# Optimization experiments

Hardware: AMD Instinct MI355X
Metric: run time of the kernel (lower is better)

## Reference

```python
import jax, jax.numpy as jnp
import numpy as np

B, L, D = 8, 2048, 512


def setup_inputs() -> dict:
    key = jax.random.key(0)
    ks = jax.random.split(key, 6)
    s = 0.02
    return {
        "q": jax.random.normal(ks[0], (B, L, D), jnp.float32),
        "k": jax.random.normal(ks[1], (B, L, D), jnp.float32),
        "v": jax.random.normal(ks[2], (B, L, D), jnp.float32),
        "Wq": jax.random.normal(ks[3], (D, D), jnp.float32) * s,
        "bq": jnp.zeros((D,), jnp.float32),
        "Wk": jax.random.normal(ks[4], (D, D), jnp.float32) * s,
        "bk": jnp.zeros((D,), jnp.float32),
        "Wv": jax.random.normal(ks[5], (D, D), jnp.float32) * s,
        "bv": jnp.zeros((D,), jnp.float32),
    }


def reference(q, k, v, Wq, bq, Wk, bk, Wv, bv):
    # Linear projections (torch Linear: x @ W.T + b)
    qp = jnp.einsum("bld,ed->ble", q, Wq) + bq
    kp = jnp.einsum("bld,ed->ble", k, Wk) + bk
    vp = jnp.einsum("bld,ed->ble", v, Wv) + bv
    # attn[b, i, j] = qp[b, i] . kp[b, j]   (no 1/sqrt(d) scaling in source)
    attn = jnp.einsum("bqd,bkd->bqk", qp, kp)
    # Faithful to torch.nn.Softmax(dim=1): normalize over the QUERY axis.
    attn = jax.nn.softmax(attn, axis=1)
    out = jnp.einsum("bqk,bkd->bqd", attn, vp)
    return out
```

## Files before the change

kernel.cpp:

```cpp
#include <hip/hip_runtime.h>
#include <math.h>


#define TKK 32

typedef __attribute__((ext_vector_type(8))) short bf16x8;
typedef __attribute__((ext_vector_type(4))) float floatx4;

typedef __attribute__((address_space(3))) short lds_short;
typedef const __attribute__((address_space(1))) short glob_short;

__device__ __forceinline__ short f2bf(float x) {
    unsigned u = __float_as_uint(x);
    u += 0x7fff + ((u >> 16) & 1);
    return (short)(u >> 16);
}
__device__ __forceinline__ float bf2f(short s) {
    return __uint_as_float(((unsigned)(unsigned short)s) << 16);
}
__device__ __forceinline__ float exp2_fast(float x) {
    float r;
    asm("v_exp_f32 %0, %1" : "=v"(r) : "v"(x));
    return r;
}

#define STAGE_SC(lane) ((((lane) & 3) ^ (((lane) >> 3) & 3)) * 8)
#define FRAG_FC(lane) (((((lane) >> 4) ^ (((lane) >> 1) & 3))) * 8)

__global__ __launch_bounds__(256) void prep(
    const float* __restrict__ q, const float* __restrict__ k,
    const float* __restrict__ v,
    const float* __restrict__ Wq, const float* __restrict__ Wk,
    const float* __restrict__ Wv,
    short* __restrict__ q_bf, short* __restrict__ k_bf, short* __restrict__ v_bf,
    short* __restrict__ Wq_bf, short* __restrict__ Wk_bf, short* __restrict__ Wv_bf,
    float* __restrict__ colsum)
{
    const int b = blockIdx.x;
    const float* in = nullptr;
    short* out = nullptr;
    long long i;
    if (b < 12288) {
        const int z = b >> 12;
        in  = (z == 0) ? q    : (z == 1) ? k    : v;
        out = (z == 0) ? q_bf : (z == 1) ? k_bf : v_bf;
        i = ((long long)(b & 4095) * 256 + threadIdx.x) * 8;
    } else if (b < 12672) {
        const int z = (b - 12288) >> 7;
        in  = (z == 0) ? Wq    : (z == 1) ? Wk    : Wv;
        out = (z == 0) ? Wq_bf : (z == 1) ? Wk_bf : Wv_bf;
        i = ((long long)((b - 12288) & 127) * 256 + threadIdx.x) * 8;
    } else {
        colsum[(b - 12672) * 256 + threadIdx.x] = 0.f;
        return;
    }
    float4 x = *(const float4*)(in + i);
    float4 y = *(const float4*)(in + i + 4);
    bf16x8 r;
    r[0] = f2bf(x.x); r[1] = f2bf(x.y); r[2] = f2bf(x.z); r[3] = f2bf(x.w);
    r[4] = f2bf(y.x); r[5] = f2bf(y.y); r[6] = f2bf(y.z); r[7] = f2bf(y.w);
    *(bf16x8*)(out + i) = r;
}

template<int TMp, int TNp, int WM, int WN, int HAS_BIAS, int OUT_BF16>
__device__ __forceinline__ void gemm_body(
    const short* __restrict__ A, const short* __restrict__ B,
    const float* __restrict__ bias, void* __restrict__ C,
    int N, int K, int m0, int n0, float escale)
{
    __shared__ short As[TMp * TKK];
    __shared__ short Bs[TNp * TKK];
    constexpr int MI = TMp / (16 * WM);
    constexpr int NJ = TNp / (16 * WN);
    const int t    = threadIdx.x;
    const int wave = t >> 6;
    const int lane = t & 63;
    const int wm = (wave / WN) * (TMp / WM);
    const int wn = (wave % WN) * (TNp / WN);
    const int sr = lane >> 2;
    const int sc = STAGE_SC(lane);
    const int fc = FRAG_FC(lane);

    floatx4 acc[MI][NJ];
    #pragma unroll
    for (int i = 0; i < MI; ++i)
        #pragma unroll
        for (int j = 0; j < NJ; ++j)
            acc[i][j] = (floatx4){0.f, 0.f, 0.f, 0.f};

    for (int k0 = 0; k0 < K; k0 += TKK) {
        #pragma unroll
        for (int c = wave; c < TMp / 16; c += 4)
            __builtin_amdgcn_global_load_lds(
                (glob_short*)(A + (long long)(m0 + c * 16 + sr) * K + k0 + sc),
                (lds_short*)(As + c * 512), 16, 0, 0);
        #pragma unroll
        for (int c = wave; c < TNp / 16; c += 4)
            __builtin_amdgcn_global_load_lds(
                (glob_short*)(B + (long long)(n0 + c * 16 + sr) * K + k0 + sc),
                (lds_short*)(Bs + c * 512), 16, 0, 0);
        __syncthreads();
        bf16x8 af[MI], bfr[NJ];
        #pragma unroll
        for (int i = 0; i < MI; ++i)
            af[i] = *(const bf16x8*)&As[(wm + i * 16 + (lane & 15)) * TKK + fc];
        #pragma unroll
        for (int j = 0; j < NJ; ++j)
            bfr[j] = *(const bf16x8*)&Bs[(wn + j * 16 + (lane & 15)) * TKK + fc];
        #pragma unroll
        for (int i = 0; i < MI; ++i)
            #pragma unroll
            for (int j = 0; j < NJ; ++j)
                acc[i][j] = __builtin_amdgcn_mfma_f32_16x16x32_bf16(af[i], bfr[j], acc[i][j], 0, 0, 0);
        __syncthreads();
    }

    #pragma unroll
    for (int i = 0; i < MI; ++i) {
        const int rbase = m0 + wm + i * 16 + (lane >> 4) * 4;
        #pragma unroll
        for (int j = 0; j < NJ; ++j) {
            const int col = n0 + wn + j * 16 + (lane & 15);
            const float bb = HAS_BIAS ? bias[col] : 0.f;
            #pragma unroll
            for (int r = 0; r < 4; ++r) {
                const long long off = (long long)(rbase + r) * N + col;
                const float vvv = (acc[i][j][r] + bb) * escale;
                if (OUT_BF16) ((short*)C)[off] = f2bf(vvv);
                else          ((float*)C)[off] = vvv;
            }
        }
    }
}

__global__ __launch_bounds__(256) void proj_gemm(
    const short* __restrict__ x0, const short* __restrict__ x1, const short* __restrict__ x2,
    const short* __restrict__ w0, const short* __restrict__ w1, const short* __restrict__ w2,
    const float* __restrict__ b0, const float* __restrict__ b1, const float* __restrict__ b2,
    short* __restrict__ y0, short* __restrict__ y1, short* __restrict__ y2,
    int N, int K)
{
    const int z = blockIdx.z;
    const short* A    = (z == 0) ? x0 : (z == 1) ? x1 : x2;
    const short* B    = (z == 0) ? w0 : (z == 1) ? w1 : w2;
    const float* bias = (z == 0) ? b0 : (z == 1) ? b1 : b2;
    short*       C    = (z == 0) ? y0 : (z == 1) ? y1 : y2;
    const float esc   = (z == 0) ? 1.4426950408889634f : 1.0f;
    gemm_body<128, 128, 2, 2, 1, 1>(A, B, bias, C, N, K,
                                    blockIdx.x * 128, blockIdx.y * 128, esc);
}

__global__ __launch_bounds__(256) void pv_gemm(
    const short* __restrict__ Eg, const short* __restrict__ vpTg,
    float* __restrict__ outg, int N, int K,
    long long sA, long long sB, long long sC)
{
    __shared__ short As[2][128 * TKK];
    __shared__ short Bs[2][64 * TKK];
    const int bz = blockIdx.z;
    const short* A = Eg   + (long long)bz * sA;
    const short* B = vpTg + (long long)bz * sB;
    float*       C = outg + (long long)bz * sC;

    const int m0 = blockIdx.x * 128;
    const int n0 = blockIdx.y * 64;
    const int t    = threadIdx.x;
    const int wave = t >> 6;
    const int lane = t & 63;
    const int wm = (wave >> 1) * 64;
    const int wn = (wave & 1)  * 32;
    const int sr = lane >> 2;
    const int sc = STAGE_SC(lane);
    const int fc = FRAG_FC(lane);

    floatx4 acc[4][2];
    #pragma unroll
    for (int i = 0; i < 4; ++i)
        #pragma unroll
        for (int j = 0; j < 2; ++j)
            acc[i][j] = (floatx4){0.f, 0.f, 0.f, 0.f};

    for (int k0 = 0; k0 < K; k0 += 2 * TKK) {
        #pragma unroll
        for (int h = 0; h < 2; ++h) {
            const int kk = k0 + h * TKK;
            #pragma unroll
            for (int c = wave; c < 8; c += 4)
                __builtin_amdgcn_global_load_lds(
                    (glob_short*)(A + (long long)(m0 + c * 16 + sr) * K + kk + sc),
                    (lds_short*)(As[h] + c * 512), 16, 0, 0);
            __builtin_amdgcn_global_load_lds(
                (glob_short*)(B + (long long)(n0 + wave * 16 + sr) * K + kk + sc),
                (lds_short*)(Bs[h] + wave * 512), 16, 0, 0);
        }
        __syncthreads();
        #pragma unroll
        for (int h = 0; h < 2; ++h) {
            bf16x8 af[4], bfr[2];
            #pragma unroll
            for (int i = 0; i < 4; ++i)
                af[i] = *(const bf16x8*)&As[h][(wm + i * 16 + (lane & 15)) * TKK + fc];
            #pragma unroll
            for (int j = 0; j < 2; ++j)
                bfr[j] = *(const bf16x8*)&Bs[h][(wn + j * 16 + (lane & 15)) * TKK + fc];
            #pragma unroll
            for (int i = 0; i < 4; ++i)
                #pragma unroll
                for (int j = 0; j < 2; ++j)
                    acc[i][j] = __builtin_amdgcn_mfma_f32_16x16x32_bf16(af[i], bfr[j], acc[i][j], 0, 0, 0);
        }
        __syncthreads();
    }

    #pragma unroll
    for (int i = 0; i < 4; ++i) {
        const int rbase = m0 + wm + i * 16 + (lane >> 4) * 4;
        #pragma unroll
        for (int j = 0; j < 2; ++j) {
            const int col = n0 + wn + j * 16 + (lane & 15);
            #pragma unroll
            for (int r = 0; r < 4; ++r)
                C[(long long)(rbase + r) * N + col] = acc[i][j][r];
        }
    }
}

__global__ __launch_bounds__(256) void gemm_nt_exp_colsum(
    const short* __restrict__ A, const short* __restrict__ B,
    short* __restrict__ E, float* __restrict__ colsum,
    int N, int K, long long sA, long long sB, long long sE)
{
    __shared__ short As[2][128 * TKK];
    __shared__ short Bs[2][128 * TKK];
    __shared__ float wsum[4][64];
    const int bz = blockIdx.z;
    A += (long long)bz * sA;
    B += (long long)bz * sB;
    E += (long long)bz * sE;
    colsum += (long long)bz * N;

    const int m0 = blockIdx.x * 128;
    const int n0 = blockIdx.y * 128;
    const int t    = threadIdx.x;
    const int wave = t >> 6;
    const int lane = t & 63;
    const int wm = (wave >> 1) * 64;
    const int wn = (wave & 1)  * 64;
    const int sr = lane >> 2;
    const int sc = STAGE_SC(lane);
    const int fc = FRAG_FC(lane);

    floatx4 acc[4][4];
    #pragma unroll
    for (int i = 0; i < 4; ++i)
        #pragma unroll
        for (int j = 0; j < 4; ++j)
            acc[i][j] = (floatx4){0.f, 0.f, 0.f, 0.f};

    for (int k0 = 0; k0 < K; k0 += 2 * TKK) {
        #pragma unroll
        for (int h = 0; h < 2; ++h) {
            const int kk = k0 + h * TKK;
            #pragma unroll
            for (int it = 0; it < 2; ++it) {
                const int chunk = it * 4 + wave;
                const int r = chunk * 16 + sr;
                __builtin_amdgcn_global_load_lds(
                    (glob_short*)(A + (long long)(m0 + r) * K + kk + sc),
                    (lds_short*)(As[h] + chunk * 512), 16, 0, 0);
                __builtin_amdgcn_global_load_lds(
                    (glob_short*)(B + (long long)(n0 + r) * K + kk + sc),
                    (lds_short*)(Bs[h] + chunk * 512), 16, 0, 0);
            }
        }
        __syncthreads();
        #pragma unroll
        for (int h = 0; h < 2; ++h) {
            bf16x8 af[4], bfr[4];
            #pragma unroll
            for (int i = 0; i < 4; ++i)
                af[i] = *(const bf16x8*)&As[h][(wm + i * 16 + (lane & 15)) * TKK + fc];
            #pragma unroll
            for (int j = 0; j < 4; ++j)
                bfr[j] = *(const bf16x8*)&Bs[h][(wn + j * 16 + (lane & 15)) * TKK + fc];
            #pragma unroll
            for (int i = 0; i < 4; ++i)
                #pragma unroll
                for (int j = 0; j < 4; ++j)
                    acc[i][j] = __builtin_amdgcn_mfma_f32_16x16x32_bf16(af[i], bfr[j], acc[i][j], 0, 0, 0);
        }
        __syncthreads();
    }

    float csum[4] = {0.f, 0.f, 0.f, 0.f};
    #pragma unroll
    for (int i = 0; i < 4; ++i) {
        const int rbase = wm + i * 16 + (lane >> 4) * 4;
        #pragma unroll
        for (int j = 0; j < 4; ++j) {
            const int col = wn + j * 16 + (lane & 15);
            #pragma unroll
            for (int r = 0; r < 4; ++r) {
                const float e = exp2_fast(acc[i][j][r]);
                E[(long long)(m0 + rbase + r) * N + (n0 + col)] = f2bf(e);
                csum[j] += e;
            }
        }
    }
    #pragma unroll
    for (int j = 0; j < 4; ++j) {
        csum[j] += __shfl_xor(csum[j], 16);
        csum[j] += __shfl_xor(csum[j], 32);
    }
    if (lane < 16) {
        #pragma unroll
        for (int j = 0; j < 4; ++j)
            wsum[wave][j * 16 + lane] = csum[j];
    }
    __syncthreads();
    if (t < 128) {
        const float s = (t < 64) ? (wsum[0][t] + wsum[2][t])
                                 : (wsum[1][t - 64] + wsum[3][t - 64]);
        atomicAdd(&colsum[n0 + t], s);
    }
}

__global__ __launch_bounds__(256) void transpose_scale_bf16(
    const short* __restrict__ in, const float* __restrict__ colsum,
    short* __restrict__ out, int R, int Cc)
{
    __shared__ short tile[32][33];
    const int b = blockIdx.z;
    in  += (long long)b * R * Cc;
    out += (long long)b * R * Cc;
    colsum += (long long)b * R;
    const int c0 = blockIdx.x * 32, r0 = blockIdx.y * 32;
    const int tx = threadIdx.x & 31, ty = threadIdx.x >> 5;
    #pragma unroll
    for (int rr = ty; rr < 32; rr += 8) {
        const float rs = 1.f / colsum[r0 + rr];
        tile[rr][tx] = f2bf(bf2f(in[(long long)(r0 + rr) * Cc + c0 + tx]) * rs);
    }
    __syncthreads();
    #pragma unroll
    for (int rr = ty; rr < 32; rr += 8)
        out[(long long)(c0 + rr) * R + r0 + tx] = tile[tx][rr];
}

extern "C" void kernel_launch(void* const* d_in, const int* in_sizes, int n_in,
                              void* d_out, int out_size, void* d_ws, size_t ws_size,
                              hipStream_t stream) {
    const float* q  = (const float*)d_in[0];
    const float* k  = (const float*)d_in[1];
    const float* v  = (const float*)d_in[2];
    const float* Wq = (const float*)d_in[3];
    const float* bq = (const float*)d_in[4];
    const float* Wk = (const float*)d_in[5];
    const float* bk = (const float*)d_in[6];
    const float* Wv = (const float*)d_in[7];
    const float* bv = (const float*)d_in[8];
    float* out = (float*)d_out;

    const int Bb = 8, L = 2048, D = 512;
    const long long BLD = (long long)Bb * L * D;
    const long long BLL = (long long)Bb * L * L;
    const long long DD  = (long long)D * D;

    short* base  = (short*)d_ws;
    short* q_bf  = base;
    short* k_bf  = q_bf  + BLD;
    short* v_bf  = k_bf  + BLD;
    short* qp_bf = v_bf  + BLD;
    short* kp_bf = qp_bf + BLD;
    short* vp_bf = kp_bf + BLD;
    short* vpT   = vp_bf + BLD;
    short* Wq_bf = vpT   + BLD;
    short* Wk_bf = Wq_bf + DD;
    short* Wv_bf = Wk_bf + DD;
    short* E_bf  = Wv_bf + DD;
    float* colsum = (float*)(E_bf + BLL);

    dim3 blk(256);

    prep<<<dim3(12736), blk, 0, stream>>>(q, k, v, Wq, Wk, Wv,
                                          q_bf, k_bf, v_bf,
                                          Wq_bf, Wk_bf, Wv_bf, colsum);

    dim3 gproj((Bb * L) / 128, D / 128, 3);
    proj_gemm<<<gproj, blk, 0, stream>>>(q_bf, k_bf, v_bf,
                                         Wq_bf, Wk_bf, Wv_bf,
                                         bq, bk, bv,
                                         qp_bf, kp_bf, vp_bf, D, D);

    dim3 gS(L / 128, L / 128, Bb);
    gemm_nt_exp_colsum<<<gS, blk, 0, stream>>>(qp_bf, kp_bf, E_bf, colsum,
                                               L, D,
                                               (long long)L * D, (long long)L * D,
                                               (long long)L * L);

    dim3 gT(D / 32, L / 32, Bb);
    transpose_scale_bf16<<<gT, blk, 0, stream>>>(vp_bf, colsum, vpT, L, D);

    dim3 gO(L / 128, D / 64, Bb);
    pv_gemm<<<gO, blk, 0, stream>>>(E_bf, vpT, out, D, L,
                                    (long long)L * L, (long long)D * L,
                                    (long long)L * D);
}
```

Measured before the change: 298.0 us.

## Double-buffer LDS tiles with next-tile prefetch in all GEMM kernels

```diff
diff --git a/kernel.cpp b/kernel.cpp
--- a/kernel.cpp
+++ b/kernel.cpp
@@ -68,8 +68,8 @@
     const float* __restrict__ bias, void* __restrict__ C,
     int N, int K, int m0, int n0, float escale)
 {
-    __shared__ short As[TMp * TKK];
-    __shared__ short Bs[TNp * TKK];
+    __shared__ short As[2][TMp * TKK];
+    __shared__ short Bs[2][TNp * TKK];
     constexpr int MI = TMp / (16 * WM);
     constexpr int NJ = TNp / (16 * WN);
     const int t    = threadIdx.x;
@@ -81,38 +81,46 @@
     const int sc = STAGE_SC(lane);
     const int fc = FRAG_FC(lane);
 
-    floatx4 acc[MI][NJ];
-    #pragma unroll
-    for (int i = 0; i < MI; ++i)
-        #pragma unroll
-        for (int j = 0; j < NJ; ++j)
-            acc[i][j] = (floatx4){0.f, 0.f, 0.f, 0.f};
-
-    for (int k0 = 0; k0 < K; k0 += TKK) {
+    auto stage = [&](int buf, int k0) {
         #pragma unroll
         for (int c = wave; c < TMp / 16; c += 4)
             __builtin_amdgcn_global_load_lds(
                 (glob_short*)(A + (long long)(m0 + c * 16 + sr) * K + k0 + sc),
-                (lds_short*)(As + c * 512), 16, 0, 0);
+                (lds_short*)(As[buf] + c * 512), 16, 0, 0);
         #pragma unroll
         for (int c = wave; c < TNp / 16; c += 4)
             __builtin_amdgcn_global_load_lds(
                 (glob_short*)(B + (long long)(n0 + c * 16 + sr) * K + k0 + sc),
-                (lds_short*)(Bs + c * 512), 16, 0, 0);
-        __syncthreads();
+                (lds_short*)(Bs[buf] + c * 512), 16, 0, 0);
+    };
+
+    floatx4 acc[MI][NJ];
+    #pragma unroll
+    for (int i = 0; i < MI; ++i)
+        #pragma unroll
+        for (int j = 0; j < NJ; ++j)
+            acc[i][j] = (floatx4){0.f, 0.f, 0.f, 0.f};
+
+    const int NT = K / TKK;
+    stage(0, 0);
+    __syncthreads();
+    int cur = 0;
+    for (int tt = 0; tt < NT; ++tt) {
+        if (tt + 1 < NT) stage(cur ^ 1, (tt + 1) * TKK);
         bf16x8 af[MI], bfr[NJ];
         #pragma unroll
         for (int i = 0; i < MI; ++i)
-            af[i] = *(const bf16x8*)&As[(wm + i * 16 + (lane & 15)) * TKK + fc];
+            af[i] = *(const bf16x8*)&As[cur][(wm + i * 16 + (lane & 15)) * TKK + fc];
         #pragma unroll
         for (int j = 0; j < NJ; ++j)
-            bfr[j] = *(const bf16x8*)&Bs[(wn + j * 16 + (lane & 15)) * TKK + fc];
+            bfr[j] = *(const bf16x8*)&Bs[cur][(wn + j * 16 + (lane & 15)) * TKK + fc];
         #pragma unroll
         for (int i = 0; i < MI; ++i)
             #pragma unroll
             for (int j = 0; j < NJ; ++j)
                 acc[i][j] = __builtin_amdgcn_mfma_f32_16x16x32_bf16(af[i], bfr[j], acc[i][j], 0, 0, 0);
         __syncthreads();
+        cur ^= 1;
     }
 
     #pragma unroll
@@ -173,6 +181,17 @@
     const int sc = STAGE_SC(lane);
     const int fc = FRAG_FC(lane);
 
+    auto stage = [&](int buf, int kk) {
+        #pragma unroll
+        for (int c = wave; c < 8; c += 4)
+            __builtin_amdgcn_global_load_lds(
+                (glob_short*)(A + (long long)(m0 + c * 16 + sr) * K + kk + sc),
+                (lds_short*)(As[buf] + c * 512), 16, 0, 0);
+        __builtin_amdgcn_global_load_lds(
+            (glob_short*)(B + (long long)(n0 + wave * 16 + sr) * K + kk + sc),
+            (lds_short*)(Bs[buf] + wave * 512), 16, 0, 0);
+    };
+
     floatx4 acc[4][2];
     #pragma unroll
     for (int i = 0; i < 4; ++i)
@@ -180,36 +199,26 @@
         for (int j = 0; j < 2; ++j)
             acc[i][j] = (floatx4){0.f, 0.f, 0.f, 0.f};
 
-    for (int k0 = 0; k0 < K; k0 += 2 * TKK) {
-        #pragma unroll
-        for (int h = 0; h < 2; ++h) {
-            const int kk = k0 + h * TKK;
-            #pragma unroll
-            for (int c = wave; c < 8; c += 4)
-                __builtin_amdgcn_global_load_lds(
-                    (glob_short*)(A + (long long)(m0 + c * 16 + sr) * K + kk + sc),
-                    (lds_short*)(As[h] + c * 512), 16, 0, 0);
-            __builtin_amdgcn_global_load_lds(
-                (glob_short*)(B + (long long)(n0 + wave * 16 + sr) * K + kk + sc),
-                (lds_short*)(Bs[h] + wave * 512), 16, 0, 0);
-        }
+    const int NT = K / TKK;
+    stage(0, 0);
+    __syncthreads();
+    int cur = 0;
+    for (int tt = 0; tt < NT; ++tt) {
+        if (tt + 1 < NT) stage(cur ^ 1, (tt + 1) * TKK);
+        bf16x8 af[4], bfr[2];
+        #pragma unroll
+        for (int i = 0; i < 4; ++i)
+            af[i] = *(const bf16x8*)&As[cur][(wm + i * 16 + (lane & 15)) * TKK + fc];
+        #pragma unroll
+        for (int j = 0; j < 2; ++j)
+            bfr[j] = *(const bf16x8*)&Bs[cur][(wn + j * 16 + (lane & 15)) * TKK + fc];
+        #pragma unroll
+        for (int i = 0; i < 4; ++i)
+            #pragma unroll
+            for (int j = 0; j < 2; ++j)
+                acc[i][j] = __builtin_amdgcn_mfma_f32_16x16x32_bf16(af[i], bfr[j], acc[i][j], 0, 0, 0);
         __syncthreads();
-        #pragma unroll
-        for (int h = 0; h < 2; ++h) {
-            bf16x8 af[4], bfr[2];
-            #pragma unroll
-            for (int i = 0; i < 4; ++i)
-                af[i] = *(const bf16x8*)&As[h][(wm + i * 16 + (lane & 15)) * TKK + fc];
-            #pragma unroll
-            for (int j = 0; j < 2; ++j)
-                bfr[j] = *(const bf16x8*)&Bs[h][(wn + j * 16 + (lane & 15)) * TKK + fc];
-            #pragma unroll
-            for (int i = 0; i < 4; ++i)
-                #pragma unroll
-                for (int j = 0; j < 2; ++j)
-                    acc[i][j] = __builtin_amdgcn_mfma_f32_16x16x32_bf16(af[i], bfr[j], acc[i][j], 0, 0, 0);
-        }
-        __syncthreads();
+        cur ^= 1;
     }
 
     #pragma unroll
@@ -250,6 +259,20 @@
     const int sc = STAGE_SC(lane);
     const int fc = FRAG_FC(lane);
 
+    auto stage = [&](int buf, int kk) {
+        #pragma unroll
+        for (int it = 0; it < 2; ++it) {
+            const int chunk = it * 4 + wave;
+            const int r = chunk * 16 + sr;
+            __builtin_amdgcn_global_load_lds(
+                (glob_short*)(A + (long long)(m0 + r) * K + kk + sc),
+                (lds_short*)(As[buf] + chunk * 512), 16, 0, 0);
+            __builtin_amdgcn_global_load_lds(
+                (glob_short*)(B + (long long)(n0 + r) * K + kk + sc),
+                (lds_short*)(Bs[buf] + chunk * 512), 16, 0, 0);
+        }
+    };
+
     floatx4 acc[4][4];
     #pragma unroll
     for (int i = 0; i < 4; ++i)
@@ -257,39 +280,26 @@
         for (int j = 0; j < 4; ++j)
             acc[i][j] = (floatx4){0.f, 0.f, 0.f, 0.f};
 
-    for (int k0 = 0; k0 < K; k0 += 2 * TKK) {
-        #pragma unroll
-        for (int h = 0; h < 2; ++h) {
-            const int kk = k0 + h * TKK;
-            #pragma unroll
-            for (int it = 0; it < 2; ++it) {
-                const int chunk = it * 4 + wave;
-                const int r = chunk * 16 + sr;
-                __builtin_amdgcn_global_load_lds(
-                    (glob_short*)(A + (long long)(m0 + r) * K + kk + sc),
-                    (lds_short*)(As[h] + chunk * 512), 16, 0, 0);
-                __builtin_amdgcn_global_load_lds(
-                    (glob_short*)(B + (long long)(n0 + r) * K + kk + sc),
-                    (lds_short*)(Bs[h] + chunk * 512), 16, 0, 0);
-            }
-        }
+    const int NT = K / TKK;
+    stage(0, 0);
+    __syncthreads();
+    int cur = 0;
+    for (int tt = 0; tt < NT; ++tt) {
+        if (tt + 1 < NT) stage(cur ^ 1, (tt + 1) * TKK);
+        bf16x8 af[4], bfr[4];
+        #pragma unroll
+        for (int i = 0; i < 4; ++i)
+            af[i] = *(const bf16x8*)&As[cur][(wm + i * 16 + (lane & 15)) * TKK + fc];
+        #pragma unroll
+        for (int j = 0; j < 4; ++j)
+            bfr[j] = *(const bf16x8*)&Bs[cur][(wn + j * 16 + (lane & 15)) * TKK + fc];
+        #pragma unroll
+        for (int i = 0; i < 4; ++i)
+            #pragma unroll
+            for (int j = 0; j < 4; ++j)
+                acc[i][j] = __builtin_amdgcn_mfma_f32_16x16x32_bf16(af[i], bfr[j], acc[i][j], 0, 0, 0);
         __syncthreads();
-        #pragma unroll
-        for (int h = 0; h < 2; ++h) {
-            bf16x8 af[4], bfr[4];
-            #pragma unroll
-            for (int i = 0; i < 4; ++i)
-                af[i] = *(const bf16x8*)&As[h][(wm + i * 16 + (lane & 15)) * TKK + fc];
-            #pragma unroll
-            for (int j = 0; j < 4; ++j)
-                bfr[j] = *(const bf16x8*)&Bs[h][(wn + j * 16 + (lane & 15)) * TKK + fc];
-            #pragma unroll
-            for (int i = 0; i < 4; ++i)
-                #pragma unroll
-                for (int j = 0; j < 4; ++j)
-                    acc[i][j] = __builtin_amdgcn_mfma_f32_16x16x32_bf16(af[i], bfr[j], acc[i][j], 0, 0, 0);
-        }
-        __syncthreads();
+        cur ^= 1;
     }
 
     float csum[4] = {0.f, 0.f, 0.f, 0.f};
```

Result: slower. 314.3 us (+5.5%).
